# Kernel optimization log

Measured on AMD Instinct MI355X. Metric: run time of the kernel, lower is better.

## Reference

```python
import jax, jax.numpy as jnp
import numpy as np

B, N_KV, N_Q = 32, 4096, 8
D_INP, D_SLOT, HEADS, MLP_H = 256, 256, 4, 1024
ITERS = 3
EPS = 1e-8


def _ln(x, g, b, eps=1e-5):
    m = jnp.mean(x, axis=-1, keepdims=True)
    v = jnp.var(x, axis=-1, keepdims=True)
    return (x - m) * jax.lax.rsqrt(v + eps) * g + b


def setup_inputs() -> dict:
    key = jax.random.key(0)
    ks = jax.random.split(key, 12)
    def w(k, shape, fan_in):
        return jax.random.normal(k, shape, jnp.float32) / np.float32(np.sqrt(fan_in))
    return {
        "inputs": jax.random.normal(ks[0], (B, N_KV, D_INP), jnp.float32),
        "slots": jax.random.normal(ks[1], (B, N_Q, D_SLOT), jnp.float32),
        "ln_in_g": jnp.ones((D_INP,), jnp.float32), "ln_in_b": jnp.zeros((D_INP,), jnp.float32),
        "ln_slot_g": jnp.ones((D_SLOT,), jnp.float32), "ln_slot_b": jnp.zeros((D_SLOT,), jnp.float32),
        "ln_mlp_g": jnp.ones((D_SLOT,), jnp.float32), "ln_mlp_b": jnp.zeros((D_SLOT,), jnp.float32),
        "Wq": w(ks[2], (D_SLOT, D_SLOT), D_SLOT),
        "Wk": w(ks[3], (D_SLOT, D_INP), D_INP),
        "Wv": w(ks[4], (D_SLOT, D_INP), D_INP),
        "W_ih": w(ks[5], (3 * D_SLOT, D_SLOT), D_SLOT),
        "W_hh": w(ks[6], (3 * D_SLOT, D_SLOT), D_SLOT),
        "b_ih": jnp.zeros((3 * D_SLOT,), jnp.float32),
        "b_hh": jnp.zeros((3 * D_SLOT,), jnp.float32),
        "W1": w(ks[7], (MLP_H, D_SLOT), D_SLOT), "b1": jnp.zeros((MLP_H,), jnp.float32),
        "W2": w(ks[8], (D_SLOT, MLP_H), MLP_H), "b2": jnp.zeros((D_SLOT,), jnp.float32),
    }


def reference(inputs, slots, ln_in_g, ln_in_b, ln_slot_g, ln_slot_b, ln_mlp_g, ln_mlp_b,
              Wq, Wk, Wv, W_ih, W_hh, b_ih, b_hh, W1, b1, W2, b2):
    Bb, Nkv, _ = inputs.shape
    _, Nq, Ds = slots.shape
    hd = Ds // HEADS

    x = _ln(inputs, ln_in_g, ln_in_b)
    # k, v: [B, H, N_kv, hd]; k pre-scaled by hd**-0.5 as in the original
    k = (x @ Wk.T).reshape(Bb, Nkv, HEADS, hd).transpose(0, 2, 1, 3) * (hd ** -0.5)
    v = (x @ Wv.T).reshape(Bb, Nkv, HEADS, hd).transpose(0, 2, 1, 3)

    attn_vis = attn_temp = None
    for it in range(ITERS):
        if it == ITERS - 1:
            slots = jax.lax.stop_gradient(slots)
        slots_prev = slots
        s = _ln(slots, ln_slot_g, ln_slot_b)
        q = (s @ Wq.T).reshape(Bb, Nq, HEADS, hd).transpose(0, 2, 1, 3)  # [B,H,Nq,hd]
        logits = jnp.einsum('bhnd,bhqd->bhnq', k, q)  # [B,H,Nkv,Nq]
        # competing softmax: normalize jointly over (head, slot) per input token
        lt = logits.transpose(0, 2, 1, 3).reshape(Bb, Nkv, HEADS * Nq)
        attn = jax.nn.softmax(lt, axis=-1).reshape(Bb, Nkv, HEADS, Nq).transpose(0, 2, 1, 3)
        attn_vis = attn.sum(axis=1)   # [B, Nkv, Nq]
        attn_temp = attn_vis          # original recomputes the identical softmax; same values
        a = attn + EPS
        a = a / a.sum(axis=-2, keepdims=True)  # renormalize over N_kv
        updates = jnp.einsum('bhnq,bhnd->bhqd', a, v).transpose(0, 2, 1, 3).reshape(Bb, Nq, Ds)
        # GRU cell (torch GRUCell math)
        gx = updates @ W_ih.T + b_ih
        gh = slots_prev @ W_hh.T + b_hh
        xr, xz, xn = jnp.split(gx, 3, axis=-1)
        hr, hz, hn = jnp.split(gh, 3, axis=-1)
        r = jax.nn.sigmoid(xr + hr)
        z = jax.nn.sigmoid(xz + hz)
        n = jnp.tanh(xn + r * hn)
        slots = (1.0 - z) * n + z * slots_prev
        # MLP with residual
        m = _ln(slots, ln_mlp_g, ln_mlp_b)
        slots = slots + (jax.nn.relu(m @ W1.T + b1) @ W2.T + b2)
    return slots, attn_vis, attn_temp
```

## Files before the change

kernel.cpp:

```cpp
#include <hip/hip_runtime.h>
#include <math.h>


#define NKV   4096
#define DD    256
#define HQN   32
#define EPSR  1e-8f

#define WS_V      0
#define WS_A0     262144
#define WS_A1     263168
#define WS_C0     264192
#define WS_C1     265216
#define WS_SLOTA  266240
#define WS_SLOTB  331776
#define WS_WQT    397312
#define WS_WPGXH  462848
#define WS_WFT    856064
#define WS_WHHT   1249280
#define WS_W1T    1347584
#define WS_W2T    1478656
#define WS_RS     1609728
#define WS_RM     1740800
#define WS_VPART  1871872

typedef float f32x4 __attribute__((ext_vector_type(4)));
typedef short s16x8 __attribute__((ext_vector_type(8)));
typedef int   v2i   __attribute__((ext_vector_type(2)));

__device__ __forceinline__ unsigned bfr(float f) {
    unsigned u = __float_as_uint(f);
    return (u + 0x7fffu + ((u >> 16) & 1u)) >> 16;
}
__device__ __forceinline__ unsigned pk2(float lo, float hi) {
    return bfr(lo) | (bfr(hi) << 16);
}
__device__ __forceinline__ float bf2f(unsigned short us) {
    return __uint_as_float((unsigned)us << 16);
}
__device__ __forceinline__ float bflo(unsigned u) { return __uint_as_float(u << 16); }
__device__ __forceinline__ float bfhi(unsigned u) { return __uint_as_float(u & 0xffff0000u); }

__device__ __forceinline__ v2i tr_read(unsigned addr) {
    v2i d;
    asm volatile("ds_read_b64_tr_b16 %0, %1" : "=v"(d) : "v"(addr));
    return d;
}
__device__ __forceinline__ s16x8 mk_frag(v2i a, v2i b) {
    union { int i[4]; s16x8 s; } u;
    u.i[0] = a.x; u.i[1] = a.y; u.i[2] = b.x; u.i[3] = b.y;
    return u.s;
}

__global__ __launch_bounds__(256) void k_copy(const float* __restrict__ in,
                                              float* __restrict__ out, int n) {
    int i = blockIdx.x * 256 + threadIdx.x;
    if (i < n) out[i] = in[i];
}

__global__ __launch_bounds__(256) void k_tr(const float* __restrict__ in,
                                            float* __restrict__ out, int R, int C) {
    __shared__ float tile[32][33];
    int bx = blockIdx.x * 32, by = blockIdx.y * 32;
    int x = bx + threadIdx.x;
    for (int k = 0; k < 32; k += 8) {
        int y = by + threadIdx.y + k;
        if (x < C && y < R) tile[threadIdx.y + k][threadIdx.x] = in[(size_t)y * C + x];
    }
    __syncthreads();
    int r = by + threadIdx.x;
    for (int k = 0; k < 32; k += 8) {
        int c = bx + threadIdx.y + k;
        if (c < C && r < R) out[(size_t)c * R + r] = tile[threadIdx.x][threadIdx.y + k];
    }
}

__global__ __launch_bounds__(256) void k_wfold(
    const float* __restrict__ Wih, const float* __restrict__ Wv,
    unsigned* __restrict__ WfT2)
{
    __shared__ float wr[256];
    const int c = blockIdx.x, t = threadIdx.x;
    wr[t] = Wih[(size_t)c * 256 + t];
    __syncthreads();
    const float2* wv2 = (const float2*)Wv;
    #pragma unroll
    for (int pp = 0; pp < 2; ++pp) {
        int P = pp * 256 + t;
        int h = P >> 7, p = P & 127;
        float f0 = 0.f, f1 = 0.f;
        #pragma unroll 8
        for (int d = 0; d < 64; ++d) {
            float a = wr[h * 64 + d];
            float2 v = wv2[(size_t)(h * 64 + d) * 128 + p];
            f0 = fmaf(a, v.x, f0); f1 = fmaf(a, v.y, f1);
        }
        WfT2[(size_t)P * 768 + c] = pk2(f0, f1);
    }
}

__global__ __launch_bounds__(256) void k_trpack(
    const float* __restrict__ in, unsigned* __restrict__ out, int R, int C)
{
    const int c2 = blockIdx.x;
    const int t = threadIdx.x;
    for (int q = 0; q < R / 256; ++q) {
        int r = q * 256 + t;
        out[(size_t)c2 * R + r] = pk2(in[(size_t)r * C + 2 * c2],
                                      in[(size_t)r * C + 2 * c2 + 1]);
    }
}

__global__ __launch_bounds__(256) void k_prep(
    const float* __restrict__ slots, const float* __restrict__ g_s, const float* __restrict__ b_s,
    const float* __restrict__ wqt, const float* __restrict__ Wk,
    const float* __restrict__ g_in, const float* __restrict__ b_in,
    unsigned short* __restrict__ wp_bf, float* __restrict__ c0_g, float* __restrict__ c1_g,
    float* __restrict__ A0_g, float* __restrict__ A1_g)
{
    __shared__ float s_lds[2048];
    __shared__ float qs[512];
    __shared__ float redc[4096];
    const int t = threadIdx.x;
    const int b = blockIdx.x, h = blockIdx.y;
    const int lane = t & 63, w = t >> 6;
    const float LNS = 0.125f * 1.44269504f;

    if (h == 0 && t < 32) { A0_g[b * 32 + t] = 0.f; A1_g[b * 32 + t] = 0.f; }

    for (int r = w; r < 8; r += 4) {
        const float4 v = ((const float4*)(slots + ((size_t)b * 8 + r) * 256))[lane];
        float s0 = v.x + v.y + v.z + v.w;
        float s1 = v.x * v.x + v.y * v.y + v.z * v.z + v.w * v.w;
        #pragma unroll
        for (int o = 32; o >= 1; o >>= 1) { s0 += __shfl_xor(s0, o, 64); s1 += __shfl_xor(s1, o, 64); }
        float m = s0 * (1.f / 256.f);
        float rs = rsqrtf(s1 * (1.f / 256.f) - m * m + 1e-5f);
        float4 gg = ((const float4*)g_s)[lane];
        float4 bb = ((const float4*)b_s)[lane];
        float4 nn;
        nn.x = (v.x - m) * rs * gg.x + bb.x;
        nn.y = (v.y - m) * rs * gg.y + bb.y;
        nn.z = (v.z - m) * rs * gg.z + bb.z;
        nn.w = (v.w - m) * rs * gg.w + bb.w;
        ((float4*)(s_lds + r * 256))[lane] = nn;
    }
    __syncthreads();

    {
        const int qi0 = t >> 6, d = t & 63;
        float a0 = 0.f, a1 = 0.f;
        #pragma unroll 8
        for (int j = 0; j < 256; ++j) {
            float wv = wqt[j * 256 + h * 64 + d];
            a0 = fmaf(s_lds[qi0 * 256 + j], wv, a0);
            a1 = fmaf(s_lds[(qi0 + 4) * 256 + j], wv, a1);
        }
        qs[qi0 * 64 + d] = a0;
        qs[(qi0 + 4) * 64 + d] = a1;
    }
    __syncthreads();

    float a2[8];
    #pragma unroll
    for (int qi = 0; qi < 8; ++qi) a2[qi] = 0.f;
    #pragma unroll 4
    for (int d = 0; d < 64; ++d) {
        float wv = Wk[(size_t)(h * 64 + d) * 256 + t];
        #pragma unroll
        for (int qi = 0; qi < 8; ++qi) a2[qi] = fmaf(qs[qi * 64 + d], wv, a2[qi]);
    }
    const float gv = g_in[t], bv = b_in[t];
    #pragma unroll
    for (int qi = 0; qi < 8; ++qi) {
        float kv = LNS * a2[qi];
        float we = kv * gv;
        wp_bf[((size_t)b * HQN + h * 8 + qi) * 256 + t] = (unsigned short)bfr(we);
        redc[qi * 256 + t] = we;
        redc[2048 + qi * 256 + t] = kv * bv;
    }
    __syncthreads();
    #pragma unroll
    for (int rep = 0; rep < 2; ++rep) {
        int r = w * 2 + rep;
        float sv1 = redc[r * 256 + lane] + redc[r * 256 + 64 + lane] +
                    redc[r * 256 + 128 + lane] + redc[r * 256 + 192 + lane];
        float sv0 = redc[2048 + r * 256 + lane] + redc[2048 + r * 256 + 64 + lane] +
                    redc[2048 + r * 256 + 128 + lane] + redc[2048 + r * 256 + 192 + lane];
        #pragma unroll
        for (int o = 32; o >= 1; o >>= 1) {
            sv1 += __shfl_xor(sv1, o, 64);
            sv0 += __shfl_xor(sv0, o, 64);
        }
        if (lane == 0) {
            c1_g[b * 32 + h * 8 + r] = sv1;
            c0_g[b * 32 + h * 8 + r] = sv0;
        }
    }
}

__device__ __forceinline__ void load_x(const float* __restrict__ inp, int b, int n0,
                                       int tok_s, int seg8, float4* ld) {
    const float4* row4 = (const float4*)(inp + ((size_t)b * NKV + n0 + tok_s) * 256);
    #pragma unroll
    for (int u = 0; u < 8; ++u) ld[u] = row4[(u >> 2) * 32 + seg8 * 4 + (u & 3)];
}

__device__ __forceinline__ void pack_x(const float4* ld, char* dst, int tok_s, int seg8) {
    #pragma unroll
    for (int c = 0; c < 2; ++c) {
        int nt = seg8 + 8 * c;
        #pragma unroll
        for (int h = 0; h < 2; ++h) {
            float4 fa = ld[c * 4 + h * 2], fb = ld[c * 4 + h * 2 + 1];
            uint4 pk;
            pk.x = pk2(fa.x, fa.y); pk.y = pk2(fa.z, fa.w);
            pk.z = pk2(fb.x, fb.y); pk.w = pk2(fb.z, fb.w);
            *(uint4*)(dst + nt * 1040 + tok_s * 32 + h * 16) = pk;
        }
    }
}

__device__ __forceinline__ void calc_stats(const float4* ld, float* sb,
                                           float* __restrict__ rs_g, float* __restrict__ rm_g,
                                           int b, int n0, int tok_s, int seg8) {
    float s0 = 0.f, s1 = 0.f;
    #pragma unroll
    for (int u = 0; u < 8; ++u) {
        float4 v = ld[u];
        s0 += v.x + v.y + v.z + v.w;
        s1 = fmaf(v.x, v.x, s1); s1 = fmaf(v.y, v.y, s1);
        s1 = fmaf(v.z, v.z, s1); s1 = fmaf(v.w, v.w, s1);
    }
    s0 += __shfl_xor(s0, 1, 64); s1 += __shfl_xor(s1, 1, 64);
    s0 += __shfl_xor(s0, 2, 64); s1 += __shfl_xor(s1, 2, 64);
    s0 += __shfl_xor(s0, 4, 64); s1 += __shfl_xor(s1, 4, 64);
    float m  = s0 * (1.f / 256.f);
    float rs = rsqrtf(s1 * (1.f / 256.f) - m * m + 1e-5f);
    if (seg8 == 0) {
        sb[tok_s] = rs;
        sb[32 + tok_s] = rs * m;
        rs_g[b * 4096 + n0 + tok_s] = rs;
        rm_g[b * 4096 + n0 + tok_s] = rs * m;
    }
}

template<int NC, int STATS, int WVIS>
__global__ __launch_bounds__(256) void k_attn(
    const float* __restrict__ inp, const unsigned short* __restrict__ wp_bf,
    const float* __restrict__ c0_g, const float* __restrict__ c1_g,
    unsigned* __restrict__ vpart, float* __restrict__ A0_g, float* __restrict__ A1_g,
    float* __restrict__ rs_g, float* __restrict__ rm_g,
    float* __restrict__ out_vis, float* __restrict__ out_temp)
{
    constexpr int KBMAX = 128 / NC;
    __shared__ unsigned short xb[8320];
    __shared__ unsigned short wl[8192];
    __shared__ unsigned short pt[1024];
    __shared__ float stats[2][64];
    __shared__ float redm[64];
    __shared__ float reds[64];

    const int t = threadIdx.x;
    const int l = t & 63, w = t >> 6;
    const int g = l >> 4, li = l & 15;
    const int b = blockIdx.y, kb = blockIdx.x;

    char* xbB = (char*)xb;
    char* wlB = (char*)wl;
    char* ptB = (char*)pt;
    const int tok_s = t >> 3, seg8 = t & 7;
    const int cbase = kb * NC;

    {
        const uint4* wp4 = (const uint4*)wp_bf + ((size_t)b * 8192 + (t >> 3) * 256 + (t & 7) * 32) / 8;
        const int hq = t >> 3, sg = t & 7;
        #pragma unroll
        for (int q = 0; q < 4; ++q) {
            uint4 v = wp4[q];
            *(uint4*)(wlB + hq * 512 + (((sg * 4 + q) ^ (hq & 7)) * 16)) = v;
        }
    }

    const int Mt = w & 1, Nt = w >> 1;
    const int hqB = Nt * 16 + li;
    const float c0r = c0_g[b * 32 + hqB];
    const float c1r = c1_g[b * 32 + hqB];
    const int MtV = w >> 1, ntb = (w & 1) * 8;
    const int hqA = MtV * 16 + li;

    f32x4 av[8];
    #pragma unroll
    for (int u = 0; u < 8; ++u) av[u] = (f32x4){0.f, 0.f, 0.f, 0.f};
    float A0acc = 0.f, A1acc = 0.f;

    const unsigned xbase = (unsigned)(uintptr_t)xbB;

    {
        float4 ldA[8];
        load_x(inp, b, cbase * 32, tok_s, seg8, ldA);
        if (STATS) {
            calc_stats(ldA, &stats[0][0], rs_g, rm_g, b, cbase * 32, tok_s, seg8);
        } else {
            if (t < 32) stats[0][t] = rs_g[b * 4096 + cbase * 32 + t];
            else if (t < 64) stats[0][t] = rm_g[b * 4096 + cbase * 32 + t - 32];
        }
        pack_x(ldA, xbB, tok_s, seg8);
    }
    __syncthreads();

    #pragma unroll
    for (int ci = 0; ci < NC; ++ci) {
        const int cur = ci & 1, nxt = cur ^ 1;
        const int n0 = (cbase + ci) * 32;

        float4 ldN[8];
        if (ci < NC - 1) load_x(inp, b, n0 + 32, tok_s, seg8, ldN);
        __builtin_amdgcn_sched_barrier(0);

        f32x4 accS = (f32x4){0.f, 0.f, 0.f, 0.f};
        #pragma unroll
        for (int kk = 0; kk < 8; ++kk) {
            s16x8 af = *(const s16x8*)(xbB + (kk * 2 + (g >> 1)) * 1040 +
                                       (Mt * 16 + li) * 32 + (g & 1) * 16);
            s16x8 bf = *(const s16x8*)(wlB + hqB * 512 + (((kk * 4 + g) ^ (hqB & 7)) * 16));
            accS = __builtin_amdgcn_mfma_f32_16x16x32_bf16(af, bf, accS, 0, 0, 0);
        }

        float lg[4], rsv[4], rmv[4], mh[4], ex[4], aa[4];
        #pragma unroll
        for (int r = 0; r < 4; ++r) {
            int tokr = Mt * 16 + g * 4 + r;
            rsv[r] = stats[cur][tokr];
            rmv[r] = stats[cur][32 + tokr];
            lg[r] = fmaf(rsv[r], accS[r], fmaf(-rmv[r], c1r, c0r));
        }
        #pragma unroll
        for (int r = 0; r < 4; ++r) {
            float v = lg[r];
            v = fmaxf(v, __shfl_xor(v, 1, 64));
            v = fmaxf(v, __shfl_xor(v, 2, 64));
            v = fmaxf(v, __shfl_xor(v, 4, 64));
            v = fmaxf(v, __shfl_xor(v, 8, 64));
            mh[r] = v;
            ex[r] = exp2f(lg[r] - v);
            float s = ex[r];
            s += __shfl_xor(s, 1, 64);
            s += __shfl_xor(s, 2, 64);
            s += __shfl_xor(s, 4, 64);
            s += __shfl_xor(s, 8, 64);
            if (li == 0) {
                int tokr = Mt * 16 + g * 4 + r;
                redm[tokr * 2 + Nt] = v;
                reds[tokr * 2 + Nt] = s;
            }
        }
        __syncthreads();
        #pragma unroll
        for (int r = 0; r < 4; ++r) {
            int tokr = Mt * 16 + g * 4 + r;
            float m0 = redm[tokr * 2], m1 = redm[tokr * 2 + 1];
            float mx = fmaxf(m0, m1);
            float tot = reds[tokr * 2] * exp2f(m0 - mx) + reds[tokr * 2 + 1] * exp2f(m1 - mx);
            aa[r] = ex[r] * (exp2f(mh[r] - mx) / tot);
            A0acc += aa[r];
            A1acc = fmaf(aa[r], rmv[r], A1acc);
        }
        {
            uint2 pw;
            pw.x = pk2(aa[0] * rsv[0], aa[1] * rsv[1]);
            pw.y = pk2(aa[2] * rsv[2], aa[3] * rsv[3]);
            int tokb = Mt * 16 + g * 4;
            int slot = (tokb >> 3) ^ ((hqB >> 1) & 3);
            *(uint2*)(ptB + hqB * 64 + slot * 16 + (tokb & 7) * 2) = pw;
        }
        __syncthreads();

        if (WVIS) {
            int tk = t >> 3, q = t & 7;
            float sv = 0.f;
            #pragma unroll
            for (int h = 0; h < 4; ++h) {
                int hq = h * 8 + q;
                int slot = (tk >> 3) ^ ((hq >> 1) & 3);
                sv += bf2f(*(const unsigned short*)(ptB + hq * 64 + slot * 16 + (tk & 7) * 2));
            }
            float vv = sv / stats[cur][tk];
            size_t o = ((size_t)b * NKV + n0 + tk) * 8 + q;
            out_vis[o] = vv; out_temp[o] = vv;
        }

        if (ci < NC - 1) {
            if (STATS) {
                calc_stats(ldN, &stats[nxt][0], rs_g, rm_g, b, n0 + 32, tok_s, seg8);
            } else {
                if (t < 32) stats[nxt][t] = rs_g[b * 4096 + n0 + 32 + t];
                else if (t < 64) stats[nxt][t] = rm_g[b * 4096 + n0 + 32 + t - 32];
            }
        }

        {
            s16x8 pa = *(const s16x8*)(ptB + hqA * 64 + ((g ^ ((hqA >> 1) & 3)) * 16));
            unsigned abase = xbase + g * 256 + li * 8;
            v2i t0a = tr_read(abase + (ntb + 0) * 1040);
            v2i t0b = tr_read(abase + (ntb + 0) * 1040 + 128);
            v2i t1a = tr_read(abase + (ntb + 1) * 1040);
            v2i t1b = tr_read(abase + (ntb + 1) * 1040 + 128);
            v2i t2a = tr_read(abase + (ntb + 2) * 1040);
            v2i t2b = tr_read(abase + (ntb + 2) * 1040 + 128);
            v2i t3a = tr_read(abase + (ntb + 3) * 1040);
            v2i t3b = tr_read(abase + (ntb + 3) * 1040 + 128);
            asm volatile("s_waitcnt lgkmcnt(0)" ::: "memory");
            __builtin_amdgcn_sched_barrier(0);
            av[0] = __builtin_amdgcn_mfma_f32_16x16x32_bf16(pa, mk_frag(t0a, t0b), av[0], 0, 0, 0);
            av[1] = __builtin_amdgcn_mfma_f32_16x16x32_bf16(pa, mk_frag(t1a, t1b), av[1], 0, 0, 0);
            av[2] = __builtin_amdgcn_mfma_f32_16x16x32_bf16(pa, mk_frag(t2a, t2b), av[2], 0, 0, 0);
            av[3] = __builtin_amdgcn_mfma_f32_16x16x32_bf16(pa, mk_frag(t3a, t3b), av[3], 0, 0, 0);
            v2i t4a = tr_read(abase + (ntb + 4) * 1040);
            v2i t4b = tr_read(abase + (ntb + 4) * 1040 + 128);
            v2i t5a = tr_read(abase + (ntb + 5) * 1040);
            v2i t5b = tr_read(abase + (ntb + 5) * 1040 + 128);
            v2i t6a = tr_read(abase + (ntb + 6) * 1040);
            v2i t6b = tr_read(abase + (ntb + 6) * 1040 + 128);
            v2i t7a = tr_read(abase + (ntb + 7) * 1040);
            v2i t7b = tr_read(abase + (ntb + 7) * 1040 + 128);
            asm volatile("s_waitcnt lgkmcnt(0)" ::: "memory");
            __builtin_amdgcn_sched_barrier(0);
            av[4] = __builtin_amdgcn_mfma_f32_16x16x32_bf16(pa, mk_frag(t4a, t4b), av[4], 0, 0, 0);
            av[5] = __builtin_amdgcn_mfma_f32_16x16x32_bf16(pa, mk_frag(t5a, t5b), av[5], 0, 0, 0);
            av[6] = __builtin_amdgcn_mfma_f32_16x16x32_bf16(pa, mk_frag(t6a, t6b), av[6], 0, 0, 0);
            av[7] = __builtin_amdgcn_mfma_f32_16x16x32_bf16(pa, mk_frag(t7a, t7b), av[7], 0, 0, 0);
        }
        __syncthreads();

        if (ci < NC - 1) {
            pack_x(ldN, xbB, tok_s, seg8);
            __syncthreads();
        }
    }

    A0acc += __shfl_xor(A0acc, 16, 64); A0acc += __shfl_xor(A0acc, 32, 64);
    A1acc += __shfl_xor(A1acc, 16, 64); A1acc += __shfl_xor(A1acc, 32, 64);
    if (g == 0) {
        atomicAdd(A0_g + b * 32 + hqB, A0acc);
        atomicAdd(A1_g + b * 32 + hqB, A1acc);
    }
    {
        const size_t blk = (size_t)b * KBMAX + kb;
        #pragma unroll
        for (int r = 0; r < 4; ++r) {
            int hq = MtV * 16 + g * 4 + r;
            unsigned* vp = vpart + (blk * 32 + hq) * 128 + li;
            #pragma unroll
            for (int ip = 0; ip < 4; ++ip) {
                unsigned u = pk2(av[2 * ip][r], av[2 * ip + 1][r]);
                int jp = (ntb >> 1) + ip;
                vp[jp * 16] = u;
            }
        }
    }
}

template<int KBMAX>
__global__ __launch_bounds__(256) void k_vred(
    const unsigned* __restrict__ vpart, float* __restrict__ V_g)
{
    const int t = threadIdx.x;
    const int b = blockIdx.x;
    const int hq = blockIdx.y * 2 + (t >> 7);
    const int tl = t & 127;
    const unsigned* p = vpart + ((size_t)(b * KBMAX) * 32 + hq) * 128 + tl;
    float lo = 0.f, hi = 0.f;
    #pragma unroll 8
    for (int kb = 0; kb < KBMAX; ++kb) {
        unsigned u = p[(size_t)kb * 4096];
        lo += bflo(u); hi += bfhi(u);
    }
    const int jp = tl >> 4, li = tl & 15;
    float* vo = V_g + ((size_t)b * 32 + hq) * 256 + jp * 32 + li;
    vo[0]  = lo;
    vo[16] = hi;
}

__global__ __launch_bounds__(256) void k_gates(
    const float* __restrict__ V_g, const float* __restrict__ A0_g,
    const float* __restrict__ A1_g,
    const float* __restrict__ g_in, const float* __restrict__ b_in,
    const float* __restrict__ slot_cur,
    const unsigned* __restrict__ WfT2, const unsigned* __restrict__ WhhT2,
    float* __restrict__ gxh, float* __restrict__ slot_nxt,
    float* __restrict__ out_slots)
{
    __shared__ __align__(16) float aT[1024 * 4];
    const int t = threadIdx.x;
    const int rg = blockIdx.y;
    const int chunk = blockIdx.x;
    const int row0 = rg * 4;
    float acc0 = 0.f, acc1 = 0.f, acc2 = 0.f, acc3 = 0.f;

    if (chunk == 0) {
        #pragma unroll
        for (int rr = 0; rr < 4; ++rr) {
            slot_nxt[(size_t)(row0 + rr) * 256 + t] = 0.f;
            if (out_slots) out_slots[(size_t)(row0 + rr) * 256 + t] = 0.f;
        }
    }

    if (chunk < 3) {
        const int b = rg >> 1, qi0 = (rg & 1) * 4;
        const float gt = g_in[t], bt = b_in[t];
        #pragma unroll
        for (int kk = 0; kk < 4; ++kk) {
            float4 y4;
            #pragma unroll
            for (int rr = 0; rr < 4; ++rr) {
                int hq = kk * 8 + qi0 + rr;
                float A0 = A0_g[b * 32 + hq], A1 = A1_g[b * 32 + hq];
                float den = A0 + EPSR * (float)NKV;
                float vv = V_g[((size_t)b * 32 + hq) * 256 + t];
                float yv = (gt * (vv - A1) + bt * A0) / den;
                ((float*)&y4)[rr] = yv;
            }
            *(float4*)(aT + (kk * 256 + t) * 4) = y4;
        }
        __syncthreads();
        const unsigned* wp = WfT2 + chunk * 256 + t;
        #pragma unroll 4
        for (int k2 = 0; k2 < 512; ++k2) {
            unsigned wv = wp[(size_t)k2 * 768];
            float w0 = bflo(wv), w1 = bfhi(wv);
            float4 a0 = *(const float4*)(aT + 8 * k2);
            float4 a1 = *(const float4*)(aT + 8 * k2 + 4);
            acc0 = fmaf(a0.x, w0, acc0); acc0 = fmaf(a1.x, w1, acc0);
            acc1 = fmaf(a0.y, w0, acc1); acc1 = fmaf(a1.y, w1, acc1);
            acc2 = fmaf(a0.z, w0, acc2); acc2 = fmaf(a1.z, w1, acc2);
            acc3 = fmaf(a0.w, w0, acc3); acc3 = fmaf(a1.w, w1, acc3);
        }
        float* go = gxh + (size_t)row0 * 1536 + chunk * 256 + t;
        go[0] = acc0; go[1536] = acc1; go[3072] = acc2; go[4608] = acc3;
    } else {
        const int gc = chunk - 3;
        {
            float4 y4;
            #pragma unroll
            for (int rr = 0; rr < 4; ++rr)
                ((float*)&y4)[rr] = slot_cur[(size_t)(row0 + rr) * 256 + t];
            *(float4*)(aT + t * 4) = y4;
        }
        __syncthreads();
        const unsigned* wp = WhhT2 + gc * 256 + t;
        #pragma unroll 4
        for (int k2 = 0; k2 < 128; ++k2) {
            unsigned wv = wp[(size_t)k2 * 768];
            float w0 = bflo(wv), w1 = bfhi(wv);
            float4 a0 = *(const float4*)(aT + 8 * k2);
            float4 a1 = *(const float4*)(aT + 8 * k2 + 4);
            acc0 = fmaf(a0.x, w0, acc0); acc0 = fmaf(a1.x, w1, acc0);
            acc1 = fmaf(a0.y, w0, acc1); acc1 = fmaf(a1.y, w1, acc1);
            acc2 = fmaf(a0.z, w0, acc2); acc2 = fmaf(a1.z, w1, acc2);
            acc3 = fmaf(a0.w, w0, acc3); acc3 = fmaf(a1.w, w1, acc3);
        }
        float* go = gxh + (size_t)row0 * 1536 + 768 + gc * 256 + t;
        go[0] = acc0; go[1536] = acc1; go[3072] = acc2; go[4608] = acc3;
    }
// ... 72 lines not shown
        const float b1t = b1[chunk * 256 + t];
        h1_l[0][t] = fmaxf(acc0 + b1t, 0.f);
        h1_l[1][t] = fmaxf(acc1 + b1t, 0.f);
        h1_l[2][t] = fmaxf(acc2 + b1t, 0.f);
        h1_l[3][t] = fmaxf(acc3 + b1t, 0.f);
    }
    __syncthreads();

    {
        float o0 = 0.f, o1 = 0.f, o2 = 0.f, o3 = 0.f;
        const unsigned* wp = W2T2 + (size_t)(chunk * 128) * 256 + t;
        #pragma unroll 4
        for (int k2 = 0; k2 < 128; ++k2) {
            unsigned wv = wp[(size_t)k2 * 256];
            float w0 = bflo(wv), w1 = bfhi(wv);
            float a00 = h1_l[0][2 * k2], a01 = h1_l[0][2 * k2 + 1];
            float a10 = h1_l[1][2 * k2], a11 = h1_l[1][2 * k2 + 1];
            float a20 = h1_l[2][2 * k2], a21 = h1_l[2][2 * k2 + 1];
            float a30 = h1_l[3][2 * k2], a31 = h1_l[3][2 * k2 + 1];
            o0 = fmaf(a00, w0, o0); o0 = fmaf(a01, w1, o0);
            o1 = fmaf(a10, w0, o1); o1 = fmaf(a11, w1, o1);
            o2 = fmaf(a20, w0, o2); o2 = fmaf(a21, w1, o2);
            o3 = fmaf(a30, w0, o3); o3 = fmaf(a31, w1, o3);
        }
        const float b2t = b2[t];
        float p0 = o0 + ((chunk == 0) ? smid[0] + b2t : 0.f);
        float p1 = o1 + ((chunk == 0) ? smid[1] + b2t : 0.f);
        float p2 = o2 + ((chunk == 0) ? smid[2] + b2t : 0.f);
        float p3 = o3 + ((chunk == 0) ? smid[3] + b2t : 0.f);
        atomicAdd(slot_nxt + (size_t)(row0 + 0) * 256 + t, p0);
        atomicAdd(slot_nxt + (size_t)(row0 + 1) * 256 + t, p1);
        atomicAdd(slot_nxt + (size_t)(row0 + 2) * 256 + t, p2);
        atomicAdd(slot_nxt + (size_t)(row0 + 3) * 256 + t, p3);
        if (out_slots) {
            atomicAdd(out_slots + (size_t)(row0 + 0) * 256 + t, p0);
            atomicAdd(out_slots + (size_t)(row0 + 1) * 256 + t, p1);
            atomicAdd(out_slots + (size_t)(row0 + 2) * 256 + t, p2);
            atomicAdd(out_slots + (size_t)(row0 + 3) * 256 + t, p3);
        }
    }
}

extern "C" void kernel_launch(void* const* d_in, const int* in_sizes, int n_in,
                              void* d_out, int out_size, void* d_ws, size_t ws_size,
                              hipStream_t stream) {
    const float* inp     = (const float*)d_in[0];
    const float* slots0  = (const float*)d_in[1];
    const float* ln_in_g = (const float*)d_in[2];
    const float* ln_in_b = (const float*)d_in[3];
    const float* ln_s_g  = (const float*)d_in[4];
    const float* ln_s_b  = (const float*)d_in[5];
    const float* ln_m_g  = (const float*)d_in[6];
    const float* ln_m_b  = (const float*)d_in[7];
    const float* Wq  = (const float*)d_in[8];
    const float* Wk  = (const float*)d_in[9];
    const float* Wv  = (const float*)d_in[10];
    const float* Wih = (const float*)d_in[11];
    const float* Whh = (const float*)d_in[12];
    const float* bih = (const float*)d_in[13];
    const float* bhh = (const float*)d_in[14];
    const float* W1  = (const float*)d_in[15];
    const float* b1  = (const float*)d_in[16];
    const float* W2  = (const float*)d_in[17];
    const float* b2  = (const float*)d_in[18];

    float* ws = (float*)d_ws;
    float* V_g   = ws + WS_V;
    float* A0_g  = ws + WS_A0;
    float* A1_g  = ws + WS_A1;
    float* c0_g  = ws + WS_C0;
    float* c1_g  = ws + WS_C1;
    float* slotA = ws + WS_SLOTA;
    float* slotB = ws + WS_SLOTB;
    float* wqt   = ws + WS_WQT;
    float* gxh   = ws + WS_WPGXH;
    unsigned short* wp_bf = (unsigned short*)(ws + WS_WPGXH);
    unsigned* WfT2  = (unsigned*)(ws + WS_WFT);
    unsigned* WhhT2 = (unsigned*)(ws + WS_WHHT);
    unsigned* W1T2  = (unsigned*)(ws + WS_W1T);
    unsigned* W2T2  = (unsigned*)(ws + WS_W2T);
    float* rs_g  = ws + WS_RS;
    float* rm_g  = ws + WS_RM;
    unsigned* vpart = (unsigned*)(ws + WS_VPART);

    float* out_slots = (float*)d_out;
    float* out_vis   = out_slots + 32 * 8 * 256;
    float* out_temp  = out_vis + 32 * 4096 * 8;

    k_tr<<<dim3(8, 8), dim3(32, 8), 0, stream>>>(Wq, wqt, 256, 256);
    k_wfold<<<768, 256, 0, stream>>>(Wih, Wv, WfT2);
    k_trpack<<<128, 256, 0, stream>>>(Whh, WhhT2, 768, 256);
    k_trpack<<<128, 256, 0, stream>>>(W1, W1T2, 1024, 256);
    k_trpack<<<512, 256, 0, stream>>>(W2, W2T2, 256, 1024);
    k_copy<<<256, 256, 0, stream>>>(slots0, slotA, 65536);

    for (int it = 0; it < 3; ++it) {
        float* cur = (it & 1) ? slotB : slotA;
        float* nxt = (it & 1) ? slotA : slotB;
        k_prep<<<dim3(32, 4), 256, 0, stream>>>(cur, ln_s_g, ln_s_b, wqt, Wk,
                                                ln_in_g, ln_in_b, wp_bf,
                                                c0_g, c1_g, A0_g, A1_g);
        if (it == 0)
            k_attn<2, 1, 0><<<dim3(64, 32), 256, 0, stream>>>(
                inp, wp_bf, c0_g, c1_g, vpart, A0_g, A1_g, rs_g, rm_g, out_vis, out_temp);
        else if (it == 1)
            k_attn<2, 0, 0><<<dim3(64, 32), 256, 0, stream>>>(
                inp, wp_bf, c0_g, c1_g, vpart, A0_g, A1_g, rs_g, rm_g, out_vis, out_temp);
        else
            k_attn<2, 0, 1><<<dim3(64, 32), 256, 0, stream>>>(
                inp, wp_bf, c0_g, c1_g, vpart, A0_g, A1_g, rs_g, rm_g, out_vis, out_temp);
        k_vred<64><<<dim3(32, 16), 256, 0, stream>>>(vpart, V_g);
        k_gates<<<dim3(6, 64), 256, 0, stream>>>(
            V_g, A0_g, A1_g, ln_in_g, ln_in_b, cur, WfT2, WhhT2, gxh, nxt,
            (it == 2) ? out_slots : nullptr);
        k_mlp<<<dim3(4, 64), 256, 0, stream>>>(
            gxh, cur, bih, bhh, ln_m_g, ln_m_b, W1T2, b1, W2T2, b2, nxt,
            (it == 2) ? out_slots : nullptr);
    }
}
```

Baseline: 452.9 us.

## Cache pre-scaled bf16 inputs across iterations and replace atomics with partial sums

The first attention pass writes bf16-packed, rs-scaled input tiles to a workspace cache. Later passes read that cache (half the bytes of the fp32 input) instead of reloading and repacking fp32, and need no per-token rs stat. The A0/A1 atomics become per-block partial sums reduced in k_vred, and s_setprio hints are placed around the MFMA blocks. The cache needs about 100MB of workspace and only turns on when ws_size is large enough. Rounding changes slightly because the rs scale is folded in before bf16 conversion.

```diff
diff --git a/kernel.cpp b/kernel.cpp
--- a/kernel.cpp
+++ b/kernel.cpp
@@ -23,6 +23,9 @@
 #define WS_RS     1609728
 #define WS_RM     1740800
 #define WS_VPART  1871872
+#define WS_APART  10260480
+#define WS_XC     10522624
+#define WS_NEED_BYTE ((size_t)(10522624 + 16777216) * 4)
 
 typedef float f32x4 __attribute__((ext_vector_type(4)));
 typedef short s16x8 __attribute__((ext_vector_type(8)));
@@ -115,8 +118,7 @@
     const float* __restrict__ slots, const float* __restrict__ g_s, const float* __restrict__ b_s,
     const float* __restrict__ wqt, const float* __restrict__ Wk,
     const float* __restrict__ g_in, const float* __restrict__ b_in,
-    unsigned short* __restrict__ wp_bf, float* __restrict__ c0_g, float* __restrict__ c1_g,
-    float* __restrict__ A0_g, float* __restrict__ A1_g)
+    unsigned short* __restrict__ wp_bf, float* __restrict__ c0_g, float* __restrict__ c1_g)
 {
     __shared__ float s_lds[2048];
     __shared__ float qs[512];
@@ -125,8 +127,6 @@
     const int b = blockIdx.x, h = blockIdx.y;
     const int lane = t & 63, w = t >> 6;
     const float LNS = 0.125f * 1.44269504f;
-
-    if (h == 0 && t < 32) { A0_g[b * 32 + t] = 0.f; A1_g[b * 32 + t] = 0.f; }
 
     for (int r = w; r < 8; r += 4) {
         const float4 v = ((const float4*)(slots + ((size_t)b * 8 + r) * 256))[lane];
@@ -206,7 +206,8 @@
     for (int u = 0; u < 8; ++u) ld[u] = row4[(u >> 2) * 32 + seg8 * 4 + (u & 3)];
 }
 
-__device__ __forceinline__ void pack_x(const float4* ld, char* dst, int tok_s, int seg8) {
+__device__ __forceinline__ void pack_x(const float4* ld, char* dst, int tok_s, int seg8,
+                                       float sc) {
     #pragma unroll
     for (int c = 0; c < 2; ++c) {
         int nt = seg8 + 8 * c;
@@ -214,16 +215,16 @@
         for (int h = 0; h < 2; ++h) {
             float4 fa = ld[c * 4 + h * 2], fb = ld[c * 4 + h * 2 + 1];
             uint4 pk;
-            pk.x = pk2(fa.x, fa.y); pk.y = pk2(fa.z, fa.w);
-            pk.z = pk2(fb.x, fb.y); pk.w = pk2(fb.z, fb.w);
+            pk.x = pk2(sc * fa.x, sc * fa.y); pk.y = pk2(sc * fa.z, sc * fa.w);
+            pk.z = pk2(sc * fb.x, sc * fb.y); pk.w = pk2(sc * fb.z, sc * fb.w);
             *(uint4*)(dst + nt * 1040 + tok_s * 32 + h * 16) = pk;
         }
     }
 }
 
-__device__ __forceinline__ void calc_stats(const float4* ld, float* sb,
-                                           float* __restrict__ rs_g, float* __restrict__ rm_g,
-                                           int b, int n0, int tok_s, int seg8) {
+__device__ __forceinline__ float calc_stats(const float4* ld, float* sb,
+                                            float* __restrict__ rs_g, float* __restrict__ rm_g,
+                                            int b, int n0, int tok_s, int seg8, int cachemode) {
     float s0 = 0.f, s1 = 0.f;
     #pragma unroll
     for (int u = 0; u < 8; ++u) {
@@ -238,19 +239,25 @@
     float m  = s0 * (1.f / 256.f);
     float rs = rsqrtf(s1 * (1.f / 256.f) - m * m + 1e-5f);
     if (seg8 == 0) {
-        sb[tok_s] = rs;
-        sb[32 + tok_s] = rs * m;
-        rs_g[b * 4096 + n0 + tok_s] = rs;
+        if (cachemode) {
+            sb[tok_s] = rs * m;
+        } else {
+            sb[tok_s] = rs;
+            sb[32 + tok_s] = rs * m;
+            rs_g[b * 4096 + n0 + tok_s] = rs;
+        }
         rm_g[b * 4096 + n0 + tok_s] = rs * m;
     }
-}
-
-template<int NC, int STATS, int WVIS>
+    return rs;
+}
+
+template<int NC, int CACHE, int STATS, int WVIS>
 __global__ __launch_bounds__(256) void k_attn(
     const float* __restrict__ inp, const unsigned short* __restrict__ wp_bf,
     const float* __restrict__ c0_g, const float* __restrict__ c1_g,
-    unsigned* __restrict__ vpart, float* __restrict__ A0_g, float* __restrict__ A1_g,
+    unsigned* __restrict__ vpart, float* __restrict__ apart,
     float* __restrict__ rs_g, float* __restrict__ rm_g,
+    uint4* __restrict__ xcache,
     float* __restrict__ out_vis, float* __restrict__ out_temp)
 {
     constexpr int KBMAX = 128 / NC;
@@ -295,30 +302,60 @@
     float A0acc = 0.f, A1acc = 0.f;
 
     const unsigned xbase = (unsigned)(uintptr_t)xbB;
-
-    {
+    const int img_ld = (0) ;
+
+    if (CACHE && !STATS) {
+        if (t < 32 * NC) stats[t >> 5][t & 31] = rm_g[b * 4096 + cbase * 32 + t];
+        uint4 cv[4];
+        const uint4* cp = xcache + (size_t)(b * 128 + cbase) * 1024;
+        #pragma unroll
+        for (int q = 0; q < 4; ++q) cv[q] = cp[q * 256 + t];
+        #pragma unroll
+        for (int q = 0; q < 4; ++q)
+            *(uint4*)(xbB + (q * 4 + w) * 1040 + l * 16) = cv[q];
+    } else {
         float4 ldA[8];
         load_x(inp, b, cbase * 32, tok_s, seg8, ldA);
+        float rs = 1.f;
         if (STATS) {
-            calc_stats(ldA, &stats[0][0], rs_g, rm_g, b, cbase * 32, tok_s, seg8);
+            rs = calc_stats(ldA, &stats[0][0], rs_g, rm_g, b, cbase * 32, tok_s, seg8, CACHE);
         } else {
             if (t < 32) stats[0][t] = rs_g[b * 4096 + cbase * 32 + t];
             else if (t < 64) stats[0][t] = rm_g[b * 4096 + cbase * 32 + t - 32];
         }
-        pack_x(ldA, xbB, tok_s, seg8);
+        pack_x(ldA, xbB, tok_s, seg8, CACHE ? rs : 1.f);
     }
     __syncthreads();
 
     #pragma unroll
     for (int ci = 0; ci < NC; ++ci) {
         const int cur = ci & 1, nxt = cur ^ 1;
+        const int sidx = (CACHE && !STATS) ? ci : cur;
         const int n0 = (cbase + ci) * 32;
+        const int cid = b * 128 + cbase + ci;
 
         float4 ldN[8];
-        if (ci < NC - 1) load_x(inp, b, n0 + 32, tok_s, seg8, ldN);
+        uint4 cvN[4];
+        if (ci < NC - 1) {
+            if (CACHE && !STATS) {
+                const uint4* cp = xcache + (size_t)(cid + 1) * 1024;
+                #pragma unroll
+                for (int q = 0; q < 4; ++q) cvN[q] = cp[q * 256 + t];
+            } else {
+                load_x(inp, b, n0 + 32, tok_s, seg8, ldN);
+            }
+        }
         __builtin_amdgcn_sched_barrier(0);
 
+        if (CACHE && STATS) {
+            uint4* cp = xcache + (size_t)cid * 1024;
+            #pragma unroll
+            for (int q = 0; q < 4; ++q)
+                cp[q * 256 + t] = *(const uint4*)(xbB + (q * 4 + w) * 1040 + l * 16);
+        }
+
         f32x4 accS = (f32x4){0.f, 0.f, 0.f, 0.f};
+        __builtin_amdgcn_s_setprio(1);
         #pragma unroll
         for (int kk = 0; kk < 8; ++kk) {
             s16x8 af = *(const s16x8*)(xbB + (kk * 2 + (g >> 1)) * 1040 +
@@ -326,14 +363,20 @@
             s16x8 bf = *(const s16x8*)(wlB + hqB * 512 + (((kk * 4 + g) ^ (hqB & 7)) * 16));
             accS = __builtin_amdgcn_mfma_f32_16x16x32_bf16(af, bf, accS, 0, 0, 0);
         }
+        __builtin_amdgcn_s_setprio(0);
 
         float lg[4], rsv[4], rmv[4], mh[4], ex[4], aa[4];
         #pragma unroll
         for (int r = 0; r < 4; ++r) {
             int tokr = Mt * 16 + g * 4 + r;
-            rsv[r] = stats[cur][tokr];
-            rmv[r] = stats[cur][32 + tokr];
-            lg[r] = fmaf(rsv[r], accS[r], fmaf(-rmv[r], c1r, c0r));
+            if (CACHE) {
+                rmv[r] = stats[sidx][tokr];
+                lg[r] = accS[r] - rmv[r] * c1r + c0r;
+            } else {
+                rsv[r] = stats[sidx][tokr];
+                rmv[r] = stats[sidx][32 + tokr];
+                lg[r] = fmaf(rsv[r], accS[r], fmaf(-rmv[r], c1r, c0r));
+            }
         }
         #pragma unroll
         for (int r = 0; r < 4; ++r) {
@@ -368,8 +411,13 @@
         }
         {
             uint2 pw;
-            pw.x = pk2(aa[0] * rsv[0], aa[1] * rsv[1]);
-            pw.y = pk2(aa[2] * rsv[2], aa[3] * rsv[3]);
+            if (CACHE) {
+                pw.x = pk2(aa[0], aa[1]);
+                pw.y = pk2(aa[2], aa[3]);
+            } else {
+                pw.x = pk2(aa[0] * rsv[0], aa[1] * rsv[1]);
+                pw.y = pk2(aa[2] * rsv[2], aa[3] * rsv[3]);
+            }
             int tokb = Mt * 16 + g * 4;
             int slot = (tokb >> 3) ^ ((hqB >> 1) & 3);
             *(uint2*)(ptB + hqB * 64 + slot * 16 + (tokb & 7) * 2) = pw;
@@ -385,15 +433,16 @@
                 int slot = (tk >> 3) ^ ((hq >> 1) & 3);
                 sv += bf2f(*(const unsigned short*)(ptB + hq * 64 + slot * 16 + (tk & 7) * 2));
             }
-            float vv = sv / stats[cur][tk];
+            float vv = CACHE ? sv : sv / stats[sidx][tk];
             size_t o = ((size_t)b * NKV + n0 + tk) * 8 + q;
             out_vis[o] = vv; out_temp[o] = vv;
         }
 
+        float rsN = 1.f;
         if (ci < NC - 1) {
             if (STATS) {
-                calc_stats(ldN, &stats[nxt][0], rs_g, rm_g, b, n0 + 32, tok_s, seg8);
-            } else {
+                rsN = calc_stats(ldN, &stats[nxt][0], rs_g, rm_g, b, n0 + 32, tok_s, seg8, CACHE);
+            } else if (!CACHE) {
                 if (t < 32) stats[nxt][t] = rs_g[b * 4096 + n0 + 32 + t];
                 else if (t < 64) stats[nxt][t] = rm_g[b * 4096 + n0 + 32 + t - 32];
             }
@@ -412,10 +461,12 @@
             v2i t3b = tr_read(abase + (ntb + 3) * 1040 + 128);
             asm volatile("s_waitcnt lgkmcnt(0)" ::: "memory");
             __builtin_amdgcn_sched_barrier(0);
+            __builtin_amdgcn_s_setprio(1);
             av[0] = __builtin_amdgcn_mfma_f32_16x16x32_bf16(pa, mk_frag(t0a, t0b), av[0], 0, 0, 0);
             av[1] = __builtin_amdgcn_mfma_f32_16x16x32_bf16(pa, mk_frag(t1a, t1b), av[1], 0, 0, 0);
             av[2] = __builtin_amdgcn_mfma_f32_16x16x32_bf16(pa, mk_frag(t2a, t2b), av[2], 0, 0, 0);
             av[3] = __builtin_amdgcn_mfma_f32_16x16x32_bf16(pa, mk_frag(t3a, t3b), av[3], 0, 0, 0);
+            __builtin_amdgcn_s_setprio(0);
             v2i t4a = tr_read(abase + (ntb + 4) * 1040);
             v2i t4b = tr_read(abase + (ntb + 4) * 1040 + 128);
             v2i t5a = tr_read(abase + (ntb + 5) * 1040);
@@ -426,27 +477,35 @@
             v2i t7b = tr_read(abase + (ntb + 7) * 1040 + 128);
             asm volatile("s_waitcnt lgkmcnt(0)" ::: "memory");
             __builtin_amdgcn_sched_barrier(0);
+            __builtin_amdgcn_s_setprio(1);
             av[4] = __builtin_amdgcn_mfma_f32_16x16x32_bf16(pa, mk_frag(t4a, t4b), av[4], 0, 0, 0);
             av[5] = __builtin_amdgcn_mfma_f32_16x16x32_bf16(pa, mk_frag(t5a, t5b), av[5], 0, 0, 0);
             av[6] = __builtin_amdgcn_mfma_f32_16x16x32_bf16(pa, mk_frag(t6a, t6b), av[6], 0, 0, 0);
             av[7] = __builtin_amdgcn_mfma_f32_16x16x32_bf16(pa, mk_frag(t7a, t7b), av[7], 0, 0, 0);
+            __builtin_amdgcn_s_setprio(0);
         }
         __syncthreads();
 
         if (ci < NC - 1) {
-            pack_x(ldN, xbB, tok_s, seg8);
+            if (CACHE && !STATS) {
+                #pragma unroll
+                for (int q = 0; q < 4; ++q)
+                    *(uint4*)(xbB + (q * 4 + w) * 1040 + l * 16) = cvN[q];
+            } else {
+                pack_x(ldN, xbB, tok_s, seg8, CACHE ? rsN : 1.f);
+            }
             __syncthreads();
         }
     }
 
     A0acc += __shfl_xor(A0acc, 16, 64); A0acc += __shfl_xor(A0acc, 32, 64);
     A1acc += __shfl_xor(A1acc, 16, 64); A1acc += __shfl_xor(A1acc, 32, 64);
+    const size_t blk = (size_t)b * KBMAX + kb;
     if (g == 0) {
-        atomicAdd(A0_g + b * 32 + hqB, A0acc);
-        atomicAdd(A1_g + b * 32 + hqB, A1acc);
+        apart[blk * 128 + Mt * 64 + hqB] = A0acc;
+        apart[blk * 128 + Mt * 64 + 32 + hqB] = A1acc;
     }
     {
-        const size_t blk = (size_t)b * KBMAX + kb;
         #pragma unroll
         for (int r = 0; r < 4; ++r) {
             int hq = MtV * 16 + g * 4 + r;
@@ -463,7 +522,8 @@
 
 template<int KBMAX>
 __global__ __launch_bounds__(256) void k_vred(
-    const unsigned* __restrict__ vpart, float* __restrict__ V_g)
+    const unsigned* __restrict__ vpart, const float* __restrict__ apart,
+    float* __restrict__ V_g, float* __restrict__ A0_g, float* __restrict__ A1_g)
 {
     const int t = threadIdx.x;
     const int b = blockIdx.x;
@@ -480,6 +540,16 @@
     float* vo = V_g + ((size_t)b * 32 + hq) * 256 + jp * 32 + li;
     vo[0]  = lo;
     vo[16] = hi;
+
+    if (blockIdx.y == 0 && t < 64) {
+        float s = 0.f;
+        const float* ap = apart + (size_t)(b * KBMAX) * 128 + t;
+        #pragma unroll 8
+        for (int kb = 0; kb < KBMAX; ++kb)
+            s += ap[(size_t)kb * 128] + ap[(size_t)kb * 128 + 64];
+        if (t < 32) A0_g[b * 32 + t] = s;
+        else        A1_g[b * 32 + t - 32] = s;
+    }
 }
 
 __global__ __launch_bounds__(256) void k_gates(
@@ -718,6 +788,10 @@
     float* rs_g  = ws + WS_RS;
     float* rm_g  = ws + WS_RM;
     unsigned* vpart = (unsigned*)(ws + WS_VPART);
+    float* apart = ws + WS_APART;
+    uint4* xcache = (uint4*)(ws + WS_XC);
+
+    const int useCache = (ws_size >= WS_NEED_BYTE) ? 1 : 0;
 
     float* out_slots = (float*)d_out;
     float* out_vis   = out_slots + 32 * 8 * 256;
@@ -734,18 +808,29 @@
         float* cur = (it & 1) ? slotB : slotA;
         float* nxt = (it & 1) ? slotA : slotB;
         k_prep<<<dim3(32, 4), 256, 0, stream>>>(cur, ln_s_g, ln_s_b, wqt, Wk,
-                                                ln_in_g, ln_in_b, wp_bf,
-                                                c0_g, c1_g, A0_g, A1_g);
-        if (it == 0)
-            k_attn<2, 1, 0><<<dim3(64, 32), 256, 0, stream>>>(
-                inp, wp_bf, c0_g, c1_g, vpart, A0_g, A1_g, rs_g, rm_g, out_vis, out_temp);
-        else if (it == 1)
-            k_attn<2, 0, 0><<<dim3(64, 32), 256, 0, stream>>>(
-                inp, wp_bf, c0_g, c1_g, vpart, A0_g, A1_g, rs_g, rm_g, out_vis, out_temp);
-        else
-            k_attn<2, 0, 1><<<dim3(64, 32), 256, 0, stream>>>(
-                inp, wp_bf, c0_g, c1_g, vpart, A0_g, A1_g, rs_g, rm_g, out_vis, out_temp);
-        k_vred<64><<<dim3(32, 16), 256, 0, stream>>>(vpart, V_g);
+                                                ln_in_g, ln_in_b, wp_bf, c0_g, c1_g);
+        if (useCache) {
+            if (it == 0)
+                k_attn<2, 1, 1, 0><<<dim3(64, 32), 256, 0, stream>>>(
+                    inp, wp_bf, c0_g, c1_g, vpart, apart, rs_g, rm_g, xcache, out_vis, out_temp);
+            else if (it == 1)
+                k_attn<2, 1, 0, 0><<<dim3(64, 32), 256, 0, stream>>>(
+                    inp, wp_bf, c0_g, c1_g, vpart, apart, rs_g, rm_g, xcache, out_vis, out_temp);
+            else
+                k_attn<2, 1, 0, 1><<<dim3(64, 32), 256, 0, stream>>>(
+                    inp, wp_bf, c0_g, c1_g, vpart, apart, rs_g, rm_g, xcache, out_vis, out_temp);
+        } else {
+            if (it == 0)
+                k_attn<2, 0, 1, 0><<<dim3(64, 32), 256, 0, stream>>>(
+                    inp, wp_bf, c0_g, c1_g, vpart, apart, rs_g, rm_g, xcache, out_vis, out_temp);
+            else if (it == 1)
+                k_attn<2, 0, 0, 0><<<dim3(64, 32), 256, 0, stream>>>(
+                    inp, wp_bf, c0_g, c1_g, vpart, apart, rs_g, rm_g, xcache, out_vis, out_temp);
+            else
+                k_attn<2, 0, 0, 1><<<dim3(64, 32), 256, 0, stream>>>(
+                    inp, wp_bf, c0_g, c1_g, vpart, apart, rs_g, rm_g, xcache, out_vis, out_temp);
+        }
+        k_vred<64><<<dim3(32, 16), 256, 0, stream>>>(vpart, apart, V_g, A0_g, A1_g);
         k_gates<<<dim3(6, 64), 256, 0, stream>>>(
             V_g, A0_g, A1_g, ln_in_g, ln_in_b, cur, WfT2, WhhT2, gxh, nxt,
             (it == 2) ? out_slots : nullptr);
```

After: 462.5 us. 2.1% more time.

## Compute full softmax per wave redundantly; replace A atomics with partial buffers

Applied to the files above, without the earlier changes.

Each wave now computes logits for both head-slot halves with two MFMA chains, so it can do the joint softmax across all 32 columns locally. This removes the LDS max/sum exchange and the __syncthreads that used to sit between the two wave groups. The per-block A0/A1 sums are written to a partial buffer and reduced in k_vred, replacing global atomics and the zeroing in k_prep. s_setprio hints are also added around the MFMA bursts. The cost is doubled QK MFMA work and extra workspace traffic.

```diff
diff --git a/kernel.cpp b/kernel.cpp
--- a/kernel.cpp
+++ b/kernel.cpp
@@ -23,6 +23,7 @@
 #define WS_RS     1609728
 #define WS_RM     1740800
 #define WS_VPART  1871872
+#define WS_APART  10260480
 
 typedef float f32x4 __attribute__((ext_vector_type(4)));
 typedef short s16x8 __attribute__((ext_vector_type(8)));
@@ -115,8 +116,7 @@
     const float* __restrict__ slots, const float* __restrict__ g_s, const float* __restrict__ b_s,
     const float* __restrict__ wqt, const float* __restrict__ Wk,
     const float* __restrict__ g_in, const float* __restrict__ b_in,
-    unsigned short* __restrict__ wp_bf, float* __restrict__ c0_g, float* __restrict__ c1_g,
-    float* __restrict__ A0_g, float* __restrict__ A1_g)
+    unsigned short* __restrict__ wp_bf, float* __restrict__ c0_g, float* __restrict__ c1_g)
 {
     __shared__ float s_lds[2048];
     __shared__ float qs[512];
@@ -125,8 +125,6 @@
     const int b = blockIdx.x, h = blockIdx.y;
     const int lane = t & 63, w = t >> 6;
     const float LNS = 0.125f * 1.44269504f;
-
-    if (h == 0 && t < 32) { A0_g[b * 32 + t] = 0.f; A1_g[b * 32 + t] = 0.f; }
 
     for (int r = w; r < 8; r += 4) {
         const float4 v = ((const float4*)(slots + ((size_t)b * 8 + r) * 256))[lane];
@@ -249,7 +247,7 @@
 __global__ __launch_bounds__(256) void k_attn(
     const float* __restrict__ inp, const unsigned short* __restrict__ wp_bf,
     const float* __restrict__ c0_g, const float* __restrict__ c1_g,
-    unsigned* __restrict__ vpart, float* __restrict__ A0_g, float* __restrict__ A1_g,
+    unsigned* __restrict__ vpart, float* __restrict__ apart,
     float* __restrict__ rs_g, float* __restrict__ rm_g,
     float* __restrict__ out_vis, float* __restrict__ out_temp)
 {
@@ -258,8 +256,6 @@
     __shared__ unsigned short wl[8192];
     __shared__ unsigned short pt[1024];
     __shared__ float stats[2][64];
-    __shared__ float redm[64];
-    __shared__ float reds[64];
 
     const int t = threadIdx.x;
     const int l = t & 63, w = t >> 6;
@@ -284,8 +280,9 @@
 
     const int Mt = w & 1, Nt = w >> 1;
     const int hqB = Nt * 16 + li;
-    const float c0r = c0_g[b * 32 + hqB];
-    const float c1r = c1_g[b * 32 + hqB];
+    const int hq0 = li, hq1 = 16 + li;
+    const float c0h0 = c0_g[b * 32 + hq0], c1h0 = c1_g[b * 32 + hq0];
+    const float c0h1 = c0_g[b * 32 + hq1], c1h1 = c1_g[b * 32 + hq1];
     const int MtV = w >> 1, ntb = (w & 1) * 8;
     const int hqA = MtV * 16 + li;
 
@@ -318,58 +315,50 @@
         if (ci < NC - 1) load_x(inp, b, n0 + 32, tok_s, seg8, ldN);
         __builtin_amdgcn_sched_barrier(0);
 
-        f32x4 accS = (f32x4){0.f, 0.f, 0.f, 0.f};
+        f32x4 accS0 = (f32x4){0.f, 0.f, 0.f, 0.f};
+        f32x4 accS1 = (f32x4){0.f, 0.f, 0.f, 0.f};
+        __builtin_amdgcn_s_setprio(1);
         #pragma unroll
         for (int kk = 0; kk < 8; ++kk) {
             s16x8 af = *(const s16x8*)(xbB + (kk * 2 + (g >> 1)) * 1040 +
                                        (Mt * 16 + li) * 32 + (g & 1) * 16);
-            s16x8 bf = *(const s16x8*)(wlB + hqB * 512 + (((kk * 4 + g) ^ (hqB & 7)) * 16));
-            accS = __builtin_amdgcn_mfma_f32_16x16x32_bf16(af, bf, accS, 0, 0, 0);
-        }
-
-        float lg[4], rsv[4], rmv[4], mh[4], ex[4], aa[4];
+            s16x8 bf0 = *(const s16x8*)(wlB + hq0 * 512 + (((kk * 4 + g) ^ (hq0 & 7)) * 16));
+            s16x8 bf1 = *(const s16x8*)(wlB + hq1 * 512 + (((kk * 4 + g) ^ (hq1 & 7)) * 16));
+            accS0 = __builtin_amdgcn_mfma_f32_16x16x32_bf16(af, bf0, accS0, 0, 0, 0);
+            accS1 = __builtin_amdgcn_mfma_f32_16x16x32_bf16(af, bf1, accS1, 0, 0, 0);
+        }
+        __builtin_amdgcn_s_setprio(0);
+
+        float aaW[4], rsv[4], rmv[4];
         #pragma unroll
         for (int r = 0; r < 4; ++r) {
             int tokr = Mt * 16 + g * 4 + r;
             rsv[r] = stats[cur][tokr];
             rmv[r] = stats[cur][32 + tokr];
-            lg[r] = fmaf(rsv[r], accS[r], fmaf(-rmv[r], c1r, c0r));
-        }
-        #pragma unroll
-        for (int r = 0; r < 4; ++r) {
-            float v = lg[r];
+            float lg0 = fmaf(rsv[r], accS0[r], fmaf(-rmv[r], c1h0, c0h0));
+            float lg1 = fmaf(rsv[r], accS1[r], fmaf(-rmv[r], c1h1, c0h1));
+            float v = fmaxf(lg0, lg1);
             v = fmaxf(v, __shfl_xor(v, 1, 64));
             v = fmaxf(v, __shfl_xor(v, 2, 64));
             v = fmaxf(v, __shfl_xor(v, 4, 64));
             v = fmaxf(v, __shfl_xor(v, 8, 64));
-            mh[r] = v;
-            ex[r] = exp2f(lg[r] - v);
-            float s = ex[r];
+            float ex0 = exp2f(lg0 - v);
+            float ex1 = exp2f(lg1 - v);
+            float s = ex0 + ex1;
             s += __shfl_xor(s, 1, 64);
             s += __shfl_xor(s, 2, 64);
             s += __shfl_xor(s, 4, 64);
             s += __shfl_xor(s, 8, 64);
-            if (li == 0) {
-                int tokr = Mt * 16 + g * 4 + r;
-                redm[tokr * 2 + Nt] = v;
-                reds[tokr * 2 + Nt] = s;
-            }
-        }
-        __syncthreads();
-        #pragma unroll
-        for (int r = 0; r < 4; ++r) {
-            int tokr = Mt * 16 + g * 4 + r;
-            float m0 = redm[tokr * 2], m1 = redm[tokr * 2 + 1];
-            float mx = fmaxf(m0, m1);
-            float tot = reds[tokr * 2] * exp2f(m0 - mx) + reds[tokr * 2 + 1] * exp2f(m1 - mx);
-            aa[r] = ex[r] * (exp2f(mh[r] - mx) / tot);
-            A0acc += aa[r];
-            A1acc = fmaf(aa[r], rmv[r], A1acc);
+            float inv = 1.f / s;
+            float aw = (Nt ? ex1 : ex0) * inv;
+            A0acc += aw;
+            A1acc = fmaf(aw, rmv[r], A1acc);
+            aaW[r] = aw * rsv[r];
         }
         {
             uint2 pw;
-            pw.x = pk2(aa[0] * rsv[0], aa[1] * rsv[1]);
-            pw.y = pk2(aa[2] * rsv[2], aa[3] * rsv[3]);
+            pw.x = pk2(aaW[0], aaW[1]);
+            pw.y = pk2(aaW[2], aaW[3]);
             int tokb = Mt * 16 + g * 4;
             int slot = (tokb >> 3) ^ ((hqB >> 1) & 3);
             *(uint2*)(ptB + hqB * 64 + slot * 16 + (tokb & 7) * 2) = pw;
@@ -412,10 +401,12 @@
             v2i t3b = tr_read(abase + (ntb + 3) * 1040 + 128);
             asm volatile("s_waitcnt lgkmcnt(0)" ::: "memory");
             __builtin_amdgcn_sched_barrier(0);
+            __builtin_amdgcn_s_setprio(1);
             av[0] = __builtin_amdgcn_mfma_f32_16x16x32_bf16(pa, mk_frag(t0a, t0b), av[0], 0, 0, 0);
             av[1] = __builtin_amdgcn_mfma_f32_16x16x32_bf16(pa, mk_frag(t1a, t1b), av[1], 0, 0, 0);
             av[2] = __builtin_amdgcn_mfma_f32_16x16x32_bf16(pa, mk_frag(t2a, t2b), av[2], 0, 0, 0);
             av[3] = __builtin_amdgcn_mfma_f32_16x16x32_bf16(pa, mk_frag(t3a, t3b), av[3], 0, 0, 0);
+            __builtin_amdgcn_s_setprio(0);
             v2i t4a = tr_read(abase + (ntb + 4) * 1040);
             v2i t4b = tr_read(abase + (ntb + 4) * 1040 + 128);
             v2i t5a = tr_read(abase + (ntb + 5) * 1040);
@@ -426,10 +417,12 @@
             v2i t7b = tr_read(abase + (ntb + 7) * 1040 + 128);
             asm volatile("s_waitcnt lgkmcnt(0)" ::: "memory");
             __builtin_amdgcn_sched_barrier(0);
+            __builtin_amdgcn_s_setprio(1);
             av[4] = __builtin_amdgcn_mfma_f32_16x16x32_bf16(pa, mk_frag(t4a, t4b), av[4], 0, 0, 0);
             av[5] = __builtin_amdgcn_mfma_f32_16x16x32_bf16(pa, mk_frag(t5a, t5b), av[5], 0, 0, 0);
             av[6] = __builtin_amdgcn_mfma_f32_16x16x32_bf16(pa, mk_frag(t6a, t6b), av[6], 0, 0, 0);
             av[7] = __builtin_amdgcn_mfma_f32_16x16x32_bf16(pa, mk_frag(t7a, t7b), av[7], 0, 0, 0);
+            __builtin_amdgcn_s_setprio(0);
         }
         __syncthreads();
 
@@ -441,12 +434,12 @@
 
     A0acc += __shfl_xor(A0acc, 16, 64); A0acc += __shfl_xor(A0acc, 32, 64);
     A1acc += __shfl_xor(A1acc, 16, 64); A1acc += __shfl_xor(A1acc, 32, 64);
+    const size_t blk = (size_t)b * KBMAX + kb;
     if (g == 0) {
-        atomicAdd(A0_g + b * 32 + hqB, A0acc);
-        atomicAdd(A1_g + b * 32 + hqB, A1acc);
+        apart[blk * 128 + Mt * 64 + hqB] = A0acc;
+        apart[blk * 128 + Mt * 64 + 32 + hqB] = A1acc;
     }
     {
-        const size_t blk = (size_t)b * KBMAX + kb;
         #pragma unroll
         for (int r = 0; r < 4; ++r) {
             int hq = MtV * 16 + g * 4 + r;
@@ -463,7 +456,8 @@
 
 template<int KBMAX>
 __global__ __launch_bounds__(256) void k_vred(
-    const unsigned* __restrict__ vpart, float* __restrict__ V_g)
+    const unsigned* __restrict__ vpart, const float* __restrict__ apart,
+    float* __restrict__ V_g, float* __restrict__ A0_g, float* __restrict__ A1_g)
 {
     const int t = threadIdx.x;
     const int b = blockIdx.x;
@@ -480,6 +474,16 @@
     float* vo = V_g + ((size_t)b * 32 + hq) * 256 + jp * 32 + li;
     vo[0]  = lo;
     vo[16] = hi;
+
+    if (blockIdx.y == 0 && t < 64) {
+        float s = 0.f;
+        const float* ap = apart + (size_t)(b * KBMAX) * 128 + t;
+        #pragma unroll 8
+        for (int kb = 0; kb < KBMAX; ++kb)
+            s += ap[(size_t)kb * 128] + ap[(size_t)kb * 128 + 64];
+        if (t < 32) A0_g[b * 32 + t] = s;
+        else        A1_g[b * 32 + t - 32] = s;
+    }
 }
 
 __global__ __launch_bounds__(256) void k_gates(
@@ -718,6 +722,7 @@
     float* rs_g  = ws + WS_RS;
     float* rm_g  = ws + WS_RM;
     unsigned* vpart = (unsigned*)(ws + WS_VPART);
+    float* apart = ws + WS_APART;
 
     float* out_slots = (float*)d_out;
     float* out_vis   = out_slots + 32 * 8 * 256;
@@ -734,18 +739,17 @@
         float* cur = (it & 1) ? slotB : slotA;
         float* nxt = (it & 1) ? slotA : slotB;
         k_prep<<<dim3(32, 4), 256, 0, stream>>>(cur, ln_s_g, ln_s_b, wqt, Wk,
-                                                ln_in_g, ln_in_b, wp_bf,
-                                                c0_g, c1_g, A0_g, A1_g);
+                                                ln_in_g, ln_in_b, wp_bf, c0_g, c1_g);
         if (it == 0)
             k_attn<2, 1, 0><<<dim3(64, 32), 256, 0, stream>>>(
-                inp, wp_bf, c0_g, c1_g, vpart, A0_g, A1_g, rs_g, rm_g, out_vis, out_temp);
+                inp, wp_bf, c0_g, c1_g, vpart, apart, rs_g, rm_g, out_vis, out_temp);
         else if (it == 1)
             k_attn<2, 0, 0><<<dim3(64, 32), 256, 0, stream>>>(
-                inp, wp_bf, c0_g, c1_g, vpart, A0_g, A1_g, rs_g, rm_g, out_vis, out_temp);
+                inp, wp_bf, c0_g, c1_g, vpart, apart, rs_g, rm_g, out_vis, out_temp);
         else
             k_attn<2, 0, 1><<<dim3(64, 32), 256, 0, stream>>>(
-                inp, wp_bf, c0_g, c1_g, vpart, A0_g, A1_g, rs_g, rm_g, out_vis, out_temp);
-        k_vred<64><<<dim3(32, 16), 256, 0, stream>>>(vpart, V_g);
+                inp, wp_bf, c0_g, c1_g, vpart, apart, rs_g, rm_g, out_vis, out_temp);
+        k_vred<64><<<dim3(32, 16), 256, 0, stream>>>(vpart, apart, V_g, A0_g, A1_g);
         k_gates<<<dim3(6, 64), 256, 0, stream>>>(
             V_g, A0_g, A1_g, ln_in_g, ln_in_b, cur, WfT2, WhhT2, gxh, nxt,
             (it == 2) ? out_slots : nullptr);
```

After: 446.3 us. About the same (-1.5%).
